# Kernel optimization log

Hardware: AMD Instinct MI355X
Metric: run time of the kernel (lower is better)

## Reference

```python
import jax, jax.numpy as jnp
import numpy as np

N_NODES = 100000
N_FEAT = 256
N_HIDDEN = 64
N_EDGES = 1600000
NEG_SLOPE = 0.05


def setup_inputs() -> dict:
    key = jax.random.key(0)
    k1, k2, k3, k4, k5 = jax.random.split(key, 5)
    x = jax.random.normal(k1, (N_NODES, N_FEAT), dtype=jnp.float32)
    W_fc = jax.random.normal(k2, (N_FEAT, N_HIDDEN), dtype=jnp.float32) * (1.0 / np.sqrt(N_FEAT))
    a_w = jax.random.normal(k3, (2 * N_HIDDEN,), dtype=jnp.float32) * (1.0 / np.sqrt(2 * N_HIDDEN))
    a_b = jax.random.normal(k4, (1,), dtype=jnp.float32) * 0.01
    edge_index = jax.random.randint(k5, (2, N_EDGES), 0, N_NODES, dtype=jnp.int64)
    return {"x": x, "W_fc": W_fc, "a_w": a_w, "a_b": a_b, "edge_index": edge_index}


def reference(x, W_fc, a_w, a_b, edge_index):
    n = x.shape[0]
    src = edge_index[0]  # row indices i
    dst = edge_index[1]  # col indices j
    Wh = x @ W_fc                                  # [N, H]
    Wh_i = Wh[src]                                  # [E, H] gather
    Wh_j = Wh[dst]                                  # [E, H] gather
    # a([Wh_i, Wh_j]) == Wh_i @ a_w[:H] + Wh_j @ a_w[H:] + a_b  (avoids materializing concat)
    H = Wh.shape[1]
    score = Wh_i @ a_w[:H] + Wh_j @ a_w[H:] + a_b[0]  # [E]
    h = jnp.exp(jax.nn.leaky_relu(score, negative_slope=NEG_SLOPE))  # [E]
    h_sum = jax.ops.segment_sum(h, src, num_segments=n)              # scatter_add over source nodes
    alpha = h / h_sum[src]                                           # edge-softmax weights
    # sparse.mm(adj_att, Wh): out[i] = sum_{(i,j) in E} alpha_ij * Wh[j]
    out = jax.ops.segment_sum(alpha[:, None] * Wh_j, src, num_segments=n)  # [N, H]
    return (out, alpha)
```

## Files before the change

kernel.cpp:

```cpp
#include <hip/hip_runtime.h>

#define N_NODES 100000
#define N_FEAT  256
#define N_HID   64
#define N_EDGES 1600000
#define NEG_SLOPE 0.05f

#define NBUCKET 391
#define TILE    2048
#define NTILES  ((N_EDGES + TILE - 1) / TILE)
#define BCAP    4704
#define BTHREADS 1024

typedef float  floatx4 __attribute__((ext_vector_type(4)));
typedef short  shortx8 __attribute__((ext_vector_type(8)));

__device__ __forceinline__ unsigned short f2bf(float f) {
  unsigned int u = __float_as_uint(f);
  u = u + 0x7fffu + ((u >> 16) & 1u);
  return (unsigned short)(u >> 16);
}
__device__ __forceinline__ float bf_lo(unsigned int u) {
  return __uint_as_float(u << 16);
}
__device__ __forceinline__ float bf_hi(unsigned int u) {
  return __uint_as_float(u & 0xFFFF0000u);
}

__global__ __launch_bounds__(256) void k_wprep(const float* __restrict__ W,
                                               unsigned short* __restrict__ WbT) {
  int n = blockIdx.x;
  int k = threadIdx.x;
  WbT[n * 256 + k] = f2bf(W[(size_t)k * N_HID + n]);
}

#define WSTRIDE 264
__global__ __launch_bounds__(256) void k_gemm(
    const float* __restrict__ x, const unsigned short* __restrict__ WbT,
    const float* __restrict__ aw, unsigned short* __restrict__ Whb,
    float* __restrict__ s1, float* __restrict__ s2) {
  __shared__ unsigned short wsm[64 * WSTRIDE];

  const int t = threadIdx.x;
  for (int idx = t; idx < 64 * 32; idx += 256) {
    int row = idx >> 5, c16 = idx & 31;
    *(uint4*)(wsm + row * WSTRIDE + c16 * 8) =
        *(const uint4*)(WbT + row * 256 + c16 * 8);
  }
  __syncthreads();

  const int w = t >> 6;
  const int lane = t & 63;
  const int q = lane >> 4;
  const int li = lane & 15;
  const int r0 = blockIdx.x * 64;
  const int grow = r0 + w * 16 + li;
  const bool vrow = grow < N_NODES;

  float4 araw[16];
  if (vrow) {
    const float4* xr = (const float4*)(x + (size_t)grow * N_FEAT);
#pragma unroll
    for (int c = 0; c < 8; ++c) {
      araw[2 * c]     = xr[c * 8 + q * 2];
      araw[2 * c + 1] = xr[c * 8 + q * 2 + 1];
    }
  } else {
#pragma unroll
    for (int i = 0; i < 16; ++i) araw[i] = make_float4(0.f, 0.f, 0.f, 0.f);
  }

  floatx4 acc[4];
#pragma unroll
  for (int g = 0; g < 4; ++g) acc[g] = (floatx4){0.f, 0.f, 0.f, 0.f};

#pragma unroll
  for (int c = 0; c < 8; ++c) {
    float4 v0 = araw[2 * c], v1 = araw[2 * c + 1];
    shortx8 a;
    a[0] = (short)f2bf(v0.x); a[1] = (short)f2bf(v0.y);
    a[2] = (short)f2bf(v0.z); a[3] = (short)f2bf(v0.w);
    a[4] = (short)f2bf(v1.x); a[5] = (short)f2bf(v1.y);
    a[6] = (short)f2bf(v1.z); a[7] = (short)f2bf(v1.w);
#pragma unroll
    for (int g = 0; g < 4; ++g) {
      shortx8 b = *(const shortx8*)(wsm + (g * 16 + li) * WSTRIDE + c * 32 + q * 8);
      acc[g] = __builtin_amdgcn_mfma_f32_16x16x32_bf16(a, b, acc[g], 0, 0, 0);
    }
  }

#pragma unroll
  for (int j = 0; j < 4; ++j) {
    int r = r0 + w * 16 + q * 4 + j;
    if (r < N_NODES) {
#pragma unroll
      for (int g = 0; g < 4; ++g)
        Whb[(size_t)r * N_HID + g * 16 + li] = f2bf(acc[g][j]);
    }
  }

#pragma unroll
  for (int j = 0; j < 4; ++j) {
    float p1 = 0.f, p2 = 0.f;
#pragma unroll
    for (int g = 0; g < 4; ++g) {
      p1 += acc[g][j] * aw[g * 16 + li];
      p2 += acc[g][j] * aw[64 + g * 16 + li];
    }
#pragma unroll
    for (int off = 1; off < 16; off <<= 1) {
      p1 += __shfl_xor(p1, off);
      p2 += __shfl_xor(p2, off);
    }
    int r = r0 + w * 16 + q * 4 + j;
    if (li == 0 && r < N_NODES) {
      s1[r] = p1;
      s2[r] = p2;
    }
  }
}

__global__ __launch_bounds__(256) void k_histT(const int* __restrict__ ei,
                                               int* __restrict__ tileCnt) {
  __shared__ int hist[NBUCKET];
  const int t = threadIdx.x;
  const int e0 = blockIdx.x * TILE;
  const int ecnt = min(TILE, N_EDGES - e0);

  for (int i = t; i < NBUCKET; i += 256) hist[i] = 0;
  __syncthreads();

#pragma unroll
  for (int j = 0; j < 8; ++j) {
    int li = j * 256 + t;
    if (li < ecnt) atomicAdd(&hist[ei[e0 + li] >> 8], 1);
  }
  __syncthreads();

  for (int b = t; b < NBUCKET; b += 256)
    tileCnt[blockIdx.x * NBUCKET + b] = hist[b];
}

__global__ __launch_bounds__(256) void k_tilescan(
    const int* __restrict__ tileCnt, int* __restrict__ tileOff,
    int* __restrict__ buckTot) {
  __shared__ int s[256];
  const int b = blockIdx.x;
  const int t = threadIdx.x;
  int running = 0;
  for (int c = 0; c < (NTILES + 255) / 256; ++c) {
    int i = c * 256 + t;
    int v = (i < NTILES) ? tileCnt[i * NBUCKET + b] : 0;
    s[t] = v;
    __syncthreads();
    for (int off = 1; off < 256; off <<= 1) {
      int tv = (t >= off) ? s[t - off] : 0;
      __syncthreads();
      s[t] += tv;
      __syncthreads();
    }
    if (i < NTILES) tileOff[i * NBUCKET + b] = running + s[t] - v;
    int tot = s[255];
    __syncthreads();
    running += tot;
  }
  if (t == 0) buckTot[b] = running;
}

__global__ __launch_bounds__(512) void k_bstart(const int* __restrict__ buckTot,
                                                int* __restrict__ buckStart) {
  __shared__ int s[512];
  int t = threadIdx.x;
  int v = (t < NBUCKET) ? buckTot[t] : 0;
  s[t] = v;
  __syncthreads();
  for (int off = 1; off < 512; off <<= 1) {
    int tv = (t >= off) ? s[t - off] : 0;
    __syncthreads();
    s[t] += tv;
    __syncthreads();
  }
  if (t < NBUCKET) buckStart[t] = s[t] - v;
  if (t == 0) buckStart[NBUCKET] = N_EDGES;
}

__global__ __launch_bounds__(256) void k_bin(
    const int* __restrict__ ei, const float* __restrict__ s1,
    const float* __restrict__ s2, const float* __restrict__ ab,
    const int* __restrict__ tileCnt, const int* __restrict__ tileOff,
    const int* __restrict__ buckStart, int2* __restrict__ binned,
    float* __restrict__ h_orig) {
  __shared__ int  hist[NBUCKET];
  __shared__ int  scanx[NBUCKET];
  __shared__ int  fillc[NBUCKET];
  __shared__ int  gbase[NBUCKET];
  __shared__ int  wsum[256];
  __shared__ int2 sorted[TILE];
  __shared__ int  tgt[TILE];

  const int t = threadIdx.x;
  const int tile = blockIdx.x;
  const int e0 = tile * TILE;
  const int ecnt = min(TILE, N_EDGES - e0);

  for (int b = t; b < NBUCKET; b += 256) {
    hist[b] = tileCnt[tile * NBUCKET + b];
    gbase[b] = buckStart[b] + tileOff[tile * NBUCKET + b];
    fillc[b] = 0;
  }
  __syncthreads();

  int b0 = t * 2, b1 = t * 2 + 1;
  int v0 = (b0 < NBUCKET) ? hist[b0] : 0;
  int v1 = (b1 < NBUCKET) ? hist[b1] : 0;
  int pairsum = v0 + v1;
  wsum[t] = pairsum;
  __syncthreads();
  for (int off = 1; off < 256; off <<= 1) {
    int tv = (t >= off) ? wsum[t - off] : 0;
    __syncthreads();
    wsum[t] += tv;
    __syncthreads();
  }
  int base = wsum[t] - pairsum;
  if (b0 < NBUCKET) scanx[b0] = base;
  if (b1 < NBUCKET) scanx[b1] = base + v0;
  __syncthreads();

  float bias = ab[0];
#pragma unroll
  for (int j = 0; j < 8; ++j) {
    int li = j * 256 + t;
    if (li < ecnt) {
      int idx = e0 + li;
      int src = ei[idx];
      int dst = ei[N_EDGES + idx];
      float sc = s1[src] + s2[dst] + bias;
      float v = sc > 0.f ? sc : NEG_SLOPE * sc;
      float h = __expf(v);
      h_orig[idx] = h;
      int b = src >> 8;
      int slot = scanx[b] + atomicAdd(&fillc[b], 1);
      sorted[slot].x = dst | ((src & 255) << 17);
      sorted[slot].y = __float_as_int(h);
      tgt[slot] = gbase[b] + (slot - scanx[b]);
    }
  }
  __syncthreads();

  for (int i = t; i < ecnt; i += 256) binned[tgt[i]] = sorted[i];
}

__global__ __launch_bounds__(BTHREADS, 8) void k_bucket(
    const int* __restrict__ buckStart, const int2* __restrict__ binned,
    const unsigned short* __restrict__ Whb, float* __restrict__ out,
    float* __restrict__ invh) {
  __shared__ int2  recs[BCAP];
  __shared__ int   startp[256];
  __shared__ int   curs[256];
  __shared__ float hsum_l[256];

  const int t = threadIdx.x;
  const int b = blockIdx.x;
  const int node0 = b * 256;
  const int W0 = buckStart[b];
  const int W1 = buckStart[b + 1];
  const int cnt = W1 - W0;

  if (t < 256) {
    curs[t] = 0;
    hsum_l[t] = 0.f;
  }
  __syncthreads();

  for (int i = t; i < cnt; i += BTHREADS) {
    int rx = binned[W0 + i].x;
    atomicAdd(&curs[(rx >> 17) & 255], 1);
  }
  __syncthreads();

  int v = 0;
  if (t < 256) {
    v = curs[t];
    startp[t] = v;
  }
  __syncthreads();
  for (int off = 1; off < 256; off <<= 1) {
    int tv = (t < 256 && t >= off) ? startp[t - off] : 0;
    __syncthreads();
    if (t < 256) startp[t] += tv;
    __syncthreads();
  }
  if (t < 256) {
    int mystart = startp[t] - v;
    startp[t] = mystart;
    curs[t] = mystart;
  }
  __syncthreads();

  for (int i = t; i < cnt; i += BTHREADS) {
    int2 r = binned[W0 + i];
    int loc = (r.x >> 17) & 255;
    int slot = atomicAdd(&curs[loc], 1);
    if (slot < BCAP) {
      recs[slot].x = r.x & 0x1FFFF;
      recs[slot].y = r.y;
    }
    atomicAdd(&hsum_l[loc], __int_as_float(r.y));
  }
  __syncthreads();

  if (t < 256) {
    int n = node0 + t;
    if (n < N_NODES) {
      float hv = hsum_l[t];
      float iv = (curs[t] > startp[t]) ? 1.f / hv : 0.f;
      invh[n] = iv;
      hsum_l[t] = iv;
    }
  }
  __syncthreads();

  const int wv = t >> 6, lane = t & 63;
  const int grp = (wv << 3) | (lane >> 3);
  const int li = lane & 7;
  for (int j = grp; j < 256; j += 128) {
    int n2 = node0 + j;
    if (n2 >= N_NODES) break;
    int beg = startp[j];
    int endp = curs[j];
    if (endp > BCAP) endp = BCAP;
    float inv = hsum_l[j];
    float acc[8] = {};
    int r = beg;
    for (; r + 4 <= endp; r += 4) {
      int2 e0 = recs[r];
      int2 e1 = recs[r + 1];
      int2 e2 = recs[r + 2];
      int2 e3 = recs[r + 3];
      uint4 w0 = *(const uint4*)(Whb + (size_t)e0.x * N_HID + li * 8);
      uint4 w1 = *(const uint4*)(Whb + (size_t)e1.x * N_HID + li * 8);
      uint4 w2 = *(const uint4*)(Whb + (size_t)e2.x * N_HID + li * 8);
      uint4 w3 = *(const uint4*)(Whb + (size_t)e3.x * N_HID + li * 8);
      float a0 = __int_as_float(e0.y) * inv;
      float a1 = __int_as_float(e1.y) * inv;
      float a2 = __int_as_float(e2.y) * inv;
      float a3 = __int_as_float(e3.y) * inv;
      acc[0] += a0 * bf_lo(w0.x); acc[1] += a0 * bf_hi(w0.x);
      acc[2] += a0 * bf_lo(w0.y); acc[3] += a0 * bf_hi(w0.y);
      acc[4] += a0 * bf_lo(w0.z); acc[5] += a0 * bf_hi(w0.z);
      acc[6] += a0 * bf_lo(w0.w); acc[7] += a0 * bf_hi(w0.w);
      acc[0] += a1 * bf_lo(w1.x); acc[1] += a1 * bf_hi(w1.x);
      acc[2] += a1 * bf_lo(w1.y); acc[3] += a1 * bf_hi(w1.y);
      acc[4] += a1 * bf_lo(w1.z); acc[5] += a1 * bf_hi(w1.z);
      acc[6] += a1 * bf_lo(w1.w); acc[7] += a1 * bf_hi(w1.w);
      acc[0] += a2 * bf_lo(w2.x); acc[1] += a2 * bf_hi(w2.x);
      acc[2] += a2 * bf_lo(w2.y); acc[3] += a2 * bf_hi(w2.y);
      acc[4] += a2 * bf_lo(w2.z); acc[5] += a2 * bf_hi(w2.z);
      acc[6] += a2 * bf_lo(w2.w); acc[7] += a2 * bf_hi(w2.w);
      acc[0] += a3 * bf_lo(w3.x); acc[1] += a3 * bf_hi(w3.x);
      acc[2] += a3 * bf_lo(w3.y); acc[3] += a3 * bf_hi(w3.y);
      acc[4] += a3 * bf_lo(w3.z); acc[5] += a3 * bf_hi(w3.z);
      acc[6] += a3 * bf_lo(w3.w); acc[7] += a3 * bf_hi(w3.w);
    }
    for (; r < endp; ++r) {
      int2 rec = recs[r];
      float a = __int_as_float(rec.y) * inv;
      uint4 wvv = *(const uint4*)(Whb + (size_t)rec.x * N_HID + li * 8);
      acc[0] += a * bf_lo(wvv.x); acc[1] += a * bf_hi(wvv.x);
      acc[2] += a * bf_lo(wvv.y); acc[3] += a * bf_hi(wvv.y);
      acc[4] += a * bf_lo(wvv.z); acc[5] += a * bf_hi(wvv.z);
      acc[6] += a * bf_lo(wvv.w); acc[7] += a * bf_hi(wvv.w);
    }
    float* op = out + (size_t)n2 * N_HID + li * 8;
    *(float4*)op = make_float4(acc[0], acc[1], acc[2], acc[3]);
    *(float4*)(op + 4) = make_float4(acc[4], acc[5], acc[6], acc[7]);
  }
}

__global__ __launch_bounds__(256) void k_alpha(
    const int* __restrict__ ei, const float* __restrict__ h_orig,
    const float* __restrict__ invh, float* __restrict__ alpha) {
  int e = blockIdx.x * 256 + threadIdx.x;
  if (e >= N_EDGES) return;
  alpha[e] = h_orig[e] * invh[ei[e]];
}

extern "C" void kernel_launch(void* const* d_in, const int* in_sizes, int n_in,
                              void* d_out, int out_size, void* d_ws,
                              size_t ws_size, hipStream_t stream) {
  const float* x  = (const float*)d_in[0];
  const float* W  = (const float*)d_in[1];
  const float* aw = (const float*)d_in[2];
  const float* ab = (const float*)d_in[3];
  const int*   ei = (const int*)d_in[4];

  float* out   = (float*)d_out;
  float* alpha = out + (size_t)N_NODES * N_HID;

  unsigned short* Whb = (unsigned short*)d_ws;
  unsigned short* WbT = Whb + (size_t)N_NODES * N_HID;
  float* s1      = (float*)(WbT + 16384);
  float* s2      = s1 + N_NODES;
  float* invh    = s2 + N_NODES;
  int2*  binned  = (int2*)(invh + N_NODES);
  float* h_orig  = (float*)(binned + N_EDGES);
  int*   tileCnt = (int*)(h_orig + N_EDGES);
  int*   tileOff = tileCnt + NTILES * NBUCKET;
  int*   buckTot = tileOff + NTILES * NBUCKET;
  int*   buckStart = buckTot + NBUCKET;

  k_wprep<<<64, 256, 0, stream>>>(W, WbT);
  k_histT<<<NTILES, 256, 0, stream>>>(ei, tileCnt);
  k_tilescan<<<NBUCKET, 256, 0, stream>>>(tileCnt, tileOff, buckTot);
  k_bstart<<<1, 512, 0, stream>>>(buckTot, buckStart);

  k_gemm<<<(N_NODES + 63) / 64, 256, 0, stream>>>(x, WbT, aw, Whb, s1, s2);

  k_bin<<<NTILES, 256, 0, stream>>>(ei, s1, s2, ab, tileCnt, tileOff,
                                    buckStart, binned, h_orig);
  k_bucket<<<NBUCKET, BTHREADS, 0, stream>>>(buckStart, binned, Whb, out, invh);
  k_alpha<<<(N_EDGES + 255) / 256, 256, 0, stream>>>(ei, h_orig, invh, alpha);
}
```

Before: 275.8 us.

## Use wave-shuffle scans and precompute per-node degree counts via global atomics

Replaces the shared-memory Hillis-Steele scans in the tile-scan, bucket-start, binning and bucket kernels with 64-lane shuffle scans plus a small per-wave total fixup, which removes many block barriers. k_tilescan now scans all tiles in a single pass with 1024 threads. Per-node edge counts are accumulated with global atomics in the histogram kernel, so the bucket kernel no longer needs its counting pass over the binned records. In exchange, the histogram kernel takes on 1.6M scattered global atomics, and the count array is zeroed inside k_wprep.

```diff
diff --git a/kernel.cpp b/kernel.cpp
--- a/kernel.cpp
+++ b/kernel.cpp
@@ -27,11 +27,23 @@
   return __uint_as_float(u & 0xFFFF0000u);
 }
 
+__device__ __forceinline__ int wave_iscan(int v, int lane) {
+#pragma unroll
+  for (int d = 1; d < 64; d <<= 1) {
+    int tv = __shfl_up(v, d);
+    if (lane >= d) v += tv;
+  }
+  return v;
+}
+
 __global__ __launch_bounds__(256) void k_wprep(const float* __restrict__ W,
-                                               unsigned short* __restrict__ WbT) {
+                                               unsigned short* __restrict__ WbT,
+                                               int* __restrict__ nodeCnt) {
   int n = blockIdx.x;
   int k = threadIdx.x;
   WbT[n * 256 + k] = f2bf(W[(size_t)k * N_HID + n]);
+  for (int i = blockIdx.x * 256 + threadIdx.x; i < N_NODES; i += 64 * 256)
+    nodeCnt[i] = 0;
 }
 
 #define WSTRIDE 264
@@ -121,7 +133,8 @@
 }
 
 __global__ __launch_bounds__(256) void k_histT(const int* __restrict__ ei,
-                                               int* __restrict__ tileCnt) {
+                                               int* __restrict__ tileCnt,
+                                               int* __restrict__ nodeCnt) {
   __shared__ int hist[NBUCKET];
   const int t = threadIdx.x;
   const int e0 = blockIdx.x * TILE;
@@ -133,7 +146,11 @@
 #pragma unroll
   for (int j = 0; j < 8; ++j) {
     int li = j * 256 + t;
-    if (li < ecnt) atomicAdd(&hist[ei[e0 + li] >> 8], 1);
+    if (li < ecnt) {
+      int s = ei[e0 + li];
+      atomicAdd(&hist[s >> 8], 1);
+      atomicAdd(&nodeCnt[s], 1);
+    }
   }
   __syncthreads();
 
@@ -141,46 +158,40 @@
     tileCnt[blockIdx.x * NBUCKET + b] = hist[b];
 }
 
-__global__ __launch_bounds__(256) void k_tilescan(
+__global__ __launch_bounds__(1024) void k_tilescan(
     const int* __restrict__ tileCnt, int* __restrict__ tileOff,
     int* __restrict__ buckTot) {
-  __shared__ int s[256];
+  __shared__ int wtot[16];
   const int b = blockIdx.x;
   const int t = threadIdx.x;
-  int running = 0;
-  for (int c = 0; c < (NTILES + 255) / 256; ++c) {
-    int i = c * 256 + t;
-    int v = (i < NTILES) ? tileCnt[i * NBUCKET + b] : 0;
-    s[t] = v;
-    __syncthreads();
-    for (int off = 1; off < 256; off <<= 1) {
-      int tv = (t >= off) ? s[t - off] : 0;
-      __syncthreads();
-      s[t] += tv;
-      __syncthreads();
-    }
-    if (i < NTILES) tileOff[i * NBUCKET + b] = running + s[t] - v;
-    int tot = s[255];
-    __syncthreads();
-    running += tot;
-  }
-  if (t == 0) buckTot[b] = running;
+  const int lane = t & 63, wv = t >> 6;
+  int v = (t < NTILES) ? tileCnt[t * NBUCKET + b] : 0;
+  int p = wave_iscan(v, lane);
+  if (lane == 63) wtot[wv] = p;
+  __syncthreads();
+  int off = 0;
+  for (int w2 = 0; w2 < wv; ++w2) off += wtot[w2];
+  if (t < NTILES) tileOff[t * NBUCKET + b] = off + p - v;
+  if (t == 0) {
+    int tot = 0;
+#pragma unroll
+    for (int w2 = 0; w2 < 16; ++w2) tot += wtot[w2];
+    buckTot[b] = tot;
+  }
 }
 
 __global__ __launch_bounds__(512) void k_bstart(const int* __restrict__ buckTot,
                                                 int* __restrict__ buckStart) {
-  __shared__ int s[512];
-  int t = threadIdx.x;
+  __shared__ int wtot[8];
+  const int t = threadIdx.x;
+  const int lane = t & 63, wv = t >> 6;
   int v = (t < NBUCKET) ? buckTot[t] : 0;
-  s[t] = v;
-  __syncthreads();
-  for (int off = 1; off < 512; off <<= 1) {
-    int tv = (t >= off) ? s[t - off] : 0;
-    __syncthreads();
-    s[t] += tv;
-    __syncthreads();
-  }
-  if (t < NBUCKET) buckStart[t] = s[t] - v;
+  int p = wave_iscan(v, lane);
+  if (lane == 63) wtot[wv] = p;
+  __syncthreads();
+  int off = 0;
+  for (int w2 = 0; w2 < wv; ++w2) off += wtot[w2];
+  if (t < NBUCKET) buckStart[t] = off + p - v;
   if (t == 0) buckStart[NBUCKET] = N_EDGES;
 }
 
@@ -194,7 +205,7 @@
   __shared__ int  scanx[NBUCKET];
   __shared__ int  fillc[NBUCKET];
   __shared__ int  gbase[NBUCKET];
-  __shared__ int  wsum[256];
+  __shared__ int  wtot[4];
   __shared__ int2 sorted[TILE];
   __shared__ int  tgt[TILE];
 
@@ -202,6 +213,7 @@
   const int tile = blockIdx.x;
   const int e0 = tile * TILE;
   const int ecnt = min(TILE, N_EDGES - e0);
+  const int lane = t & 63, wv = t >> 6;
 
   for (int b = t; b < NBUCKET; b += 256) {
     hist[b] = tileCnt[tile * NBUCKET + b];
@@ -214,15 +226,12 @@
   int v0 = (b0 < NBUCKET) ? hist[b0] : 0;
   int v1 = (b1 < NBUCKET) ? hist[b1] : 0;
   int pairsum = v0 + v1;
-  wsum[t] = pairsum;
-  __syncthreads();
-  for (int off = 1; off < 256; off <<= 1) {
-    int tv = (t >= off) ? wsum[t - off] : 0;
-    __syncthreads();
-    wsum[t] += tv;
-    __syncthreads();
-  }
-  int base = wsum[t] - pairsum;
+  int p = wave_iscan(pairsum, lane);
+  if (lane == 63) wtot[wv] = p;
+  __syncthreads();
+  int off = 0;
+  for (int w2 = 0; w2 < wv; ++w2) off += wtot[w2];
+  int base = off + p - pairsum;
   if (b0 < NBUCKET) scanx[b0] = base;
   if (b1 < NBUCKET) scanx[b1] = base + v0;
   __syncthreads();
@@ -254,45 +263,34 @@
 __global__ __launch_bounds__(BTHREADS, 8) void k_bucket(
     const int* __restrict__ buckStart, const int2* __restrict__ binned,
     const unsigned short* __restrict__ Whb, float* __restrict__ out,
-    float* __restrict__ invh) {
+    float* __restrict__ invh, const int* __restrict__ nodeCnt) {
   __shared__ int2  recs[BCAP];
   __shared__ int   startp[256];
   __shared__ int   curs[256];
   __shared__ float hsum_l[256];
-
-  const int t = threadIdx.x;
+  __shared__ int   wtot[4];
+
+  const int t = threadIdx.x;
+  const int lane = t & 63, wvx = t >> 6;
   const int b = blockIdx.x;
   const int node0 = b * 256;
   const int W0 = buckStart[b];
   const int W1 = buckStart[b + 1];
   const int cnt = W1 - W0;
 
-  if (t < 256) {
-    curs[t] = 0;
-    hsum_l[t] = 0.f;
-  }
-  __syncthreads();
-
-  for (int i = t; i < cnt; i += BTHREADS) {
-    int rx = binned[W0 + i].x;
-    atomicAdd(&curs[(rx >> 17) & 255], 1);
-  }
-  __syncthreads();
-
   int v = 0;
   if (t < 256) {
-    v = curs[t];
-    startp[t] = v;
-  }
-  __syncthreads();
-  for (int off = 1; off < 256; off <<= 1) {
-    int tv = (t < 256 && t >= off) ? startp[t - off] : 0;
-    __syncthreads();
-    if (t < 256) startp[t] += tv;
-    __syncthreads();
-  }
+    int n = node0 + t;
+    v = (n < N_NODES) ? nodeCnt[n] : 0;
+    hsum_l[t] = 0.f;
+  }
+  int p = wave_iscan(v, lane);
+  if (t < 256 && lane == 63) wtot[wvx] = p;
+  __syncthreads();
   if (t < 256) {
-    int mystart = startp[t] - v;
+    int off = 0;
+    for (int w2 = 0; w2 < wvx; ++w2) off += wtot[w2];
+    int mystart = off + p - v;
     startp[t] = mystart;
     curs[t] = mystart;
   }
@@ -314,16 +312,16 @@
     int n = node0 + t;
     if (n < N_NODES) {
       float hv = hsum_l[t];
-      float iv = (curs[t] > startp[t]) ? 1.f / hv : 0.f;
+      float iv = (v > 0) ? 1.f / hv : 0.f;
       invh[n] = iv;
       hsum_l[t] = iv;
     }
   }
   __syncthreads();
 
-  const int wv = t >> 6, lane = t & 63;
-  const int grp = (wv << 3) | (lane >> 3);
-  const int li = lane & 7;
+  const int wv = t >> 6, lane2 = t & 63;
+  const int grp = (wv << 3) | (lane2 >> 3);
+  const int li = lane2 & 7;
   for (int j = grp; j < 256; j += 128) {
     int n2 = node0 + j;
     if (n2 >= N_NODES) break;
@@ -409,16 +407,18 @@
   int*   tileOff = tileCnt + NTILES * NBUCKET;
   int*   buckTot = tileOff + NTILES * NBUCKET;
   int*   buckStart = buckTot + NBUCKET;
-
-  k_wprep<<<64, 256, 0, stream>>>(W, WbT);
-  k_histT<<<NTILES, 256, 0, stream>>>(ei, tileCnt);
-  k_tilescan<<<NBUCKET, 256, 0, stream>>>(tileCnt, tileOff, buckTot);
+  int*   nodeCnt = buckStart + NBUCKET + 1;
+
+  k_wprep<<<64, 256, 0, stream>>>(W, WbT, nodeCnt);
+  k_histT<<<NTILES, 256, 0, stream>>>(ei, tileCnt, nodeCnt);
+  k_tilescan<<<NBUCKET, 1024, 0, stream>>>(tileCnt, tileOff, buckTot);
   k_bstart<<<1, 512, 0, stream>>>(buckTot, buckStart);
 
   k_gemm<<<(N_NODES + 63) / 64, 256, 0, stream>>>(x, WbT, aw, Whb, s1, s2);
 
   k_bin<<<NTILES, 256, 0, stream>>>(ei, s1, s2, ab, tileCnt, tileOff,
                                     buckStart, binned, h_orig);
-  k_bucket<<<NBUCKET, BTHREADS, 0, stream>>>(buckStart, binned, Whb, out, invh);
+  k_bucket<<<NBUCKET, BTHREADS, 0, stream>>>(buckStart, binned, Whb, out, invh,
+                                             nodeCnt);
   k_alpha<<<(N_EDGES + 255) / 256, 256, 0, stream>>>(ei, h_orig, invh, alpha);
 }
```

Measured after the change: 331.5 us. 1.2x slower.
